# Performance work log

Measured on AMD Instinct MI355X. Metric: run time of the kernel, lower is better.

## Reference

```python
import jax, jax.numpy as jnp
import numpy as np

N_NODES = 100000
N_EDGES = 3200000
N_GRAPHS = 64


def gcn_conv(x, W, b, src, dst, num_nodes):
    # PyG GCNConv: h = x @ W; add self-loops; symmetric norm D^-1/2 (A+I) D^-1/2; bias after aggregation
    h = x @ W  # [N, out]
    loop = jnp.arange(num_nodes, dtype=src.dtype)
    src2 = jnp.concatenate([src, loop])
    dst2 = jnp.concatenate([dst, loop])
    deg = jax.ops.segment_sum(jnp.ones_like(src2, dtype=h.dtype), dst2, num_segments=num_nodes)
    dinv = jnp.where(deg > 0, jax.lax.rsqrt(jnp.maximum(deg, 1e-12)), 0.0)
    norm = dinv[src2] * dinv[dst2]  # [E+N]
    msg = h[src2] * norm[:, None]   # gather + scale (memory-bound)
    out = jax.ops.segment_sum(msg, dst2, num_segments=num_nodes)  # scatter-add
    return out + b


def global_mean_pool(x, batch, num_graphs):
    sums = jax.ops.segment_sum(x, batch, num_segments=num_graphs)
    cnts = jax.ops.segment_sum(jnp.ones((x.shape[0],), dtype=x.dtype), batch, num_segments=num_graphs)
    return sums / jnp.maximum(cnts, 1.0)[:, None]


def setup_inputs() -> dict:
    key = jax.random.key(0)
    ks = jax.random.split(key, 9)
    x = jax.random.normal(ks[0], (N_NODES, 1), dtype=jnp.float32)
    edge_index = jax.random.randint(ks[1], (2, N_EDGES), 0, N_NODES, dtype=jnp.int64)
    batch = jnp.sort(jax.random.randint(ks[2], (N_NODES,), 0, N_GRAPHS, dtype=jnp.int64))
    # Glorot-ish params
    W1 = jax.random.normal(ks[3], (1, 64), dtype=jnp.float32) * 0.5
    b1 = jnp.zeros((64,), dtype=jnp.float32)
    W2 = jax.random.normal(ks[4], (64, 32), dtype=jnp.float32) * (1.0 / np.sqrt(64))
    b2 = jnp.zeros((32,), dtype=jnp.float32)
    Wfc = jax.random.normal(ks[5], (32, 1), dtype=jnp.float32) * (1.0 / np.sqrt(32))
    bfc = jnp.zeros((1,), dtype=jnp.float32)
    return {"x": x, "edge_index": edge_index, "batch": batch,
            "W1": W1, "b1": b1, "W2": W2, "b2": b2, "Wfc": Wfc, "bfc": bfc}


def reference(x, edge_index, batch, W1, b1, W2, b2, Wfc, bfc):
    src, dst = edge_index[0], edge_index[1]
    h = jax.nn.relu(gcn_conv(x, W1, b1, src, dst, N_NODES))
    h = jax.nn.relu(gcn_conv(h, W2, b2, src, dst, N_NODES))
    g = global_mean_pool(h, batch, N_GRAPHS)  # [num_graphs, 32]
    return jax.nn.sigmoid(g @ Wfc + bfc)      # [num_graphs, 1]
```

## Files before the change

### kernel.cpp

```cpp
#include <hip/hip_runtime.h>
#include <math.h>

#define N_NODES 100000
#define N_EDGES 3200000
#define N_GRAPHS 64
#define BW 512
#define LSH 9
#define LMASK 511u
#define NBUCK ((N_NODES + BW - 1) / BW)
#define CHUNK_E 16384
#define NCHUNK ((N_EDGES + CHUNK_E - 1) / CHUNK_E)
#define CAP_E 18432
#define POOL_SCALE 1024.0f
#define POOL_INV (1.0f / 1024.0f)
#define SENT ((unsigned int)N_NODES << LSH)

__global__ void k_part(const int* __restrict__ src, const int* __restrict__ dst,
                       unsigned int* __restrict__ gcur, unsigned int* __restrict__ packed) {
    __shared__ unsigned int hist[NBUCK];
    __shared__ unsigned int sstart[NBUCK];
    for (int i = threadIdx.x; i < NBUCK; i += blockDim.x) hist[i] = 0u;
    __syncthreads();
    int e0 = blockIdx.x * CHUNK_E;
    int e1 = min(e0 + CHUNK_E, N_EDGES);
    for (int e = e0 + threadIdx.x; e < e1; e += blockDim.x)
        atomicAdd(&hist[dst[e] >> LSH], 1u);
    __syncthreads();
    for (int i = threadIdx.x; i < NBUCK; i += blockDim.x) {
        unsigned int h = hist[i];
        sstart[i] = h ? ((unsigned int)i * CAP_E + atomicAdd(&gcur[i], h)) : 0u;
        hist[i] = 0u;
    }
    __syncthreads();
    for (int e = e0 + threadIdx.x; e < e1; e += blockDim.x) {
        int d = dst[e];
        int bk = d >> LSH;
        unsigned int pos = sstart[bk] + atomicAdd(&hist[bk], 1u);
        packed[pos] = ((unsigned int)src[e] << LSH) | ((unsigned int)d & LMASK);
    }
}

__global__ void k_sorta(const unsigned int* __restrict__ gcur,
                        const unsigned int* __restrict__ packed,
                        unsigned int* __restrict__ rowstart, const float* __restrict__ x,
                        float* __restrict__ dinv, float* __restrict__ s, float2* __restrict__ ac) {
    __shared__ unsigned int hist[BW];
    __shared__ unsigned int scan[BW];
    __shared__ unsigned int sdp[256];
    __shared__ unsigned int swbase;
    int b = blockIdx.x;
    int t = threadIdx.x;
    unsigned int gv = 0u;
    if (t < 256) { gv = (t < NBUCK) ? gcur[t] : 0u; sdp[t] = gv; }
    if (t < BW) hist[t] = 0u;
    if (b == 0 && t == 0) ac[N_NODES] = make_float2(0.0f, 0.0f);
    __syncthreads();
    for (int o = 1; o < 256; o <<= 1) {
        unsigned int v = 0u;
        if (t < 256 && t >= o) v = sdp[t - o];
        __syncthreads();
        if (t < 256 && t >= o) sdp[t] += v;
        __syncthreads();
    }
    if (t == b) swbase = sdp[t] - gv;
    __syncthreads();
    unsigned int wbase = swbase;
    unsigned int r0 = (unsigned int)b * CAP_E;
    unsigned int r1 = r0 + gcur[b];
    for (unsigned int e = r0 + t; e < r1; e += blockDim.x)
        atomicAdd(&hist[packed[e] & LMASK], 1u);
    __syncthreads();
    if (t < BW) scan[t] = hist[t];
    __syncthreads();
    for (int o = 1; o < BW; o <<= 1) {
        unsigned int v = 0u;
        if (t < BW && t >= o) v = scan[t - o];
        __syncthreads();
        if (t < BW && t >= o) scan[t] += v;
        __syncthreads();
    }
    if (t < BW) {
        unsigned int deg = hist[t];
        rowstart[b * BW + t] = wbase + scan[t] - deg;
        int n = b * BW + t;
        if (n < N_NODES) {
            float di = 1.0f / sqrtf((float)(deg + 1u));
            dinv[n] = di;
            s[n] = x[n] * di;
        }
    }
}

__global__ void k_sortb(const unsigned int* __restrict__ gcur,
                        const unsigned int* __restrict__ packed,
                        const unsigned int* __restrict__ rowstart,
                        unsigned int* __restrict__ packed2,
                        const float* __restrict__ dinv, const float* __restrict__ s,
                        float2* __restrict__ ac) {
    __shared__ unsigned int cur[BW];
    __shared__ float fsum[BW];
    int b = blockIdx.x;
    unsigned int r0 = (unsigned int)b * CAP_E;
    unsigned int r1 = r0 + gcur[b];
    if (threadIdx.x < BW) {
        cur[threadIdx.x] = rowstart[b * BW + threadIdx.x];
        fsum[threadIdx.x] = 0.0f;
    }
    __syncthreads();
    for (unsigned int e = r0 + threadIdx.x; e < r1; e += blockDim.x) {
        unsigned int p = packed[e];
        unsigned int d = p & LMASK;
        unsigned int pos = atomicAdd(&cur[d], 1u);
        packed2[pos] = p;
        atomicAdd(&fsum[d], s[p >> LSH]);
    }
    __syncthreads();
    if (threadIdx.x < BW) {
        int n = b * BW + threadIdx.x;
        if (n < N_NODES) {
            float di = dinv[n];
            ac[n] = make_float2(di, di * di * (fsum[threadIdx.x] + s[n]));
        }
    }
}

#define NPW 8

#define EDGE_PAIR(P) { \
    float4 q_ = Epair4[(P)]; \
    H += fmaxf(fmaf(q_.y, w1j, q_.x * b1j), 0.0f); \
    H += fmaxf(fmaf(q_.w, w1j, q_.z * b1j), 0.0f); }

#define BLOCK16(P0) { \
    EDGE_PAIR((P0) + 0) EDGE_PAIR((P0) + 1) EDGE_PAIR((P0) + 2) EDGE_PAIR((P0) + 3) \
    EDGE_PAIR((P0) + 4) EDGE_PAIR((P0) + 5) EDGE_PAIR((P0) + 6) EDGE_PAIR((P0) + 7) }

__global__ __launch_bounds__(256, 6)
void k_l2(const unsigned int* __restrict__ rowstart, const unsigned int* __restrict__ packed2,
          const float2* __restrict__ ac,
          const float* __restrict__ W1, const float* __restrict__ b1,
          const float* __restrict__ W2, const float* __restrict__ b2,
          const int* __restrict__ batch, int* __restrict__ gsumi) {
    __shared__ float Hrow[4][64];
    __shared__ float4 Ebuf[4][32];
    const int lane = threadIdx.x & 63;
    const int wv   = threadIdx.x >> 6;
    const int k    = lane & 31;
    const int jh   = lane >> 5;
    const int j0   = jh * 32;

    const float w1j = W1[lane];
    const float b1j = b1[lane];
    const float b2k = b2[k];
    float w2c[32];
#pragma unroll
    for (int j = 0; j < 32; j++) w2c[j] = W2[(j0 + j) * 32 + k];

    float4* Epair4 = &Ebuf[wv][0];
    float2* Ewr    = (float2*)&Ebuf[wv][0];

    int n0 = (blockIdx.x * 4 + wv) * NPW;
    float racc = 0.0f;
    int curg = -1;
    for (int i = 0; i < NPW; i++) {
        int n = n0 + i;
        if (n >= N_NODES) break;
        unsigned int rs = rowstart[n], re = rowstart[n + 1];
        float2 acn = ac[n];
        float H = fmaxf(fmaf(acn.y, w1j, acn.x * b1j), 0.0f);
        unsigned int e0 = rs;
        while (e0 + 64u <= re) {
            unsigned int p = packed2[e0 + lane];
            Ewr[lane] = ac[p >> LSH];
            BLOCK16(0) BLOCK16(8) BLOCK16(16) BLOCK16(24)
            e0 += 64u;
        }
        unsigned int rem = re - e0;
        if (rem) {
            unsigned int idx = e0 + lane;
            unsigned int p = SENT;
            if (idx < re) p = packed2[idx];
            Ewr[lane] = ac[p >> LSH];
            switch ((rem + 15u) >> 4) {
                case 4: BLOCK16(24); [[fallthrough]];
                case 3: BLOCK16(16); [[fallthrough]];
                case 2: BLOCK16(8);  [[fallthrough]];
                case 1: BLOCK16(0);
            }
        }
        Hrow[wv][lane] = H;
        float accv = 0.0f;
#pragma unroll
        for (int jj = 0; jj < 8; jj++) {
            float4 hv = *(const float4*)&Hrow[wv][j0 + 4 * jj];
            accv += hv.x * w2c[4 * jj + 0] + hv.y * w2c[4 * jj + 1]
                  + hv.z * w2c[4 * jj + 2] + hv.w * w2c[4 * jj + 3];
        }
        accv += __shfl_xor(accv, 32);
        float v = fmaxf(fmaf(acn.x, accv, b2k), 0.0f);
        int gb = batch[n];
        if (gb != curg) {
            if (curg >= 0 && jh == 0)
                atomicAdd(&gsumi[curg * 32 + k], __float2int_rn(racc * POOL_SCALE));
            racc = 0.0f; curg = gb;
        }
        racc += v;
    }
    if (curg >= 0 && jh == 0)
        atomicAdd(&gsumi[curg * 32 + k], __float2int_rn(racc * POOL_SCALE));
}

__global__ void k_readout(const int* __restrict__ gsumi, const int* __restrict__ batch,
                          const float* __restrict__ Wfc, const float* __restrict__ bfc,
                          float* __restrict__ out) {
    __shared__ int lb[N_GRAPHS + 1];
    int b = threadIdx.x;
    if (b <= N_GRAPHS) {
        int lo = 0, hi = N_NODES;
        while (lo < hi) {
            int mid = (lo + hi) >> 1;
            if (batch[mid] < b) lo = mid + 1; else hi = mid;
        }
        lb[b] = lo;
    }
    __syncthreads();
    if (b < N_GRAPHS) {
        float inv = 1.0f / fmaxf((float)(lb[b + 1] - lb[b]), 1.0f);
        float acc = bfc[0];
#pragma unroll
        for (int k = 0; k < 32; k++)
            acc += (float)gsumi[b * 32 + k] * POOL_INV * inv * Wfc[k];
        out[b] = 1.0f / (1.0f + expf(-acc));
    }
}

extern "C" void kernel_launch(void* const* d_in, const int* in_sizes, int n_in,
                              void* d_out, int out_size, void* d_ws, size_t ws_size,
                              hipStream_t stream) {
    const float* x    = (const float*)d_in[0];
    const int*   ei   = (const int*)d_in[1];
    const int*   batch= (const int*)d_in[2];
    const float* W1   = (const float*)d_in[3];
    const float* b1   = (const float*)d_in[4];
    const float* W2   = (const float*)d_in[5];
    const float* b2   = (const float*)d_in[6];
    const float* Wfc  = (const float*)d_in[7];
    const float* bfc  = (const float*)d_in[8];
    float* out = (float*)d_out;

    const int* srcIdx = ei;
    const int* dstIdx = ei + N_EDGES;

    char* w = (char*)d_ws;
    unsigned int* gcur    = (unsigned int*)w; w += ((NBUCK + 64) & ~63) * 4;
    unsigned int* packed  = (unsigned int*)w; w += (size_t)NBUCK * CAP_E * 4;
    unsigned int* packed2 = (unsigned int*)w; w += (size_t)(N_EDGES + 64) * 4;
    unsigned int* rowstart= (unsigned int*)w; w += (size_t)(NBUCK * BW + 64) * 4;
    float* dinv = (float*)w;                  w += (size_t)N_NODES * 4;
    float* sbuf = (float*)w;                  w += (size_t)N_NODES * 4;
    float2* ac  = (float2*)w;                 w += (size_t)(N_NODES + 8) * 8;
    int* gsumi  = (int*)w;                    w += (size_t)N_GRAPHS * 32 * 4;

    hipMemsetAsync(gcur, 0, (size_t)NBUCK * 4, stream);
    hipMemsetAsync(gsumi, 0, (size_t)N_GRAPHS * 32 * 4, stream);

    k_part <<<NCHUNK, 1024, 0, stream>>>(srcIdx, dstIdx, gcur, packed);
    k_sorta<<<NBUCK, 1024, 0, stream>>>(gcur, packed, rowstart, x, dinv, sbuf, ac);
    k_sortb<<<NBUCK, 1024, 0, stream>>>(gcur, packed, rowstart, packed2, dinv, sbuf, ac);
    k_l2   <<<(N_NODES + 4 * NPW - 1) / (4 * NPW), 256, 0, stream>>>(rowstart, packed2, ac, W1, b1, W2, b2, batch, gsumi);
    k_readout<<<1, 128, 0, stream>>>(gsumi, batch, Wfc, bfc, out);
}
```

Baseline: 207.5 us.

## Fuse partition and two sort kernels into one cooperative kernel with grid syncs

Merges the three CSR-building kernels (bucket partition, per-bucket histogram/scan, scatter/feature sum) into one cooperatively launched kernel. Grid-wide syncs now separate the phases, relying on the partition and bucket grids being the same size (196 blocks). The aim is to remove two kernel launches and their gaps, and to keep dinv/s values in registers instead of reloading them. In exchange it needs all 196 blocks of 1024 threads resident at once, and pays for the grid-sync barriers.

```diff
diff --git a/kernel.cpp b/kernel.cpp
--- a/kernel.cpp
+++ b/kernel.cpp
@@ -1,5 +1,8 @@
 #include <hip/hip_runtime.h>
+#include <hip/hip_cooperative_groups.h>
 #include <math.h>
+
+namespace cg = cooperative_groups;
 
 #define N_NODES 100000
 #define N_EDGES 3200000
@@ -15,59 +18,63 @@
 #define POOL_INV (1.0f / 1024.0f)
 #define SENT ((unsigned int)N_NODES << LSH)
 
-__global__ void k_part(const int* __restrict__ src, const int* __restrict__ dst,
-                       unsigned int* __restrict__ gcur, unsigned int* __restrict__ packed) {
-    __shared__ unsigned int hist[NBUCK];
+__global__ __launch_bounds__(1024, 1)
+void k_build(const int* __restrict__ src, const int* __restrict__ dst,
+             unsigned int* __restrict__ gcur, unsigned int* __restrict__ packed,
+             unsigned int* __restrict__ packed2, unsigned int* __restrict__ rowstart,
+             const float* __restrict__ x, float* __restrict__ dinv, float* __restrict__ s,
+             float2* __restrict__ ac) {
+    __shared__ unsigned int h1[NBUCK];
     __shared__ unsigned int sstart[NBUCK];
-    for (int i = threadIdx.x; i < NBUCK; i += blockDim.x) hist[i] = 0u;
-    __syncthreads();
-    int e0 = blockIdx.x * CHUNK_E;
+    __shared__ unsigned int hist[BW];
+    __shared__ unsigned int scan[BW];
+    __shared__ unsigned int cur[BW];
+    __shared__ float fsum[BW];
+    __shared__ unsigned int swbase;
+    cg::grid_group grid = cg::this_grid();
+    const int b = blockIdx.x;
+    const int t = threadIdx.x;
+
+    for (int i = t; i < NBUCK; i += 1024) h1[i] = 0u;
+    __syncthreads();
+    int e0 = b * CHUNK_E;
     int e1 = min(e0 + CHUNK_E, N_EDGES);
-    for (int e = e0 + threadIdx.x; e < e1; e += blockDim.x)
-        atomicAdd(&hist[dst[e] >> LSH], 1u);
-    __syncthreads();
-    for (int i = threadIdx.x; i < NBUCK; i += blockDim.x) {
-        unsigned int h = hist[i];
-        sstart[i] = h ? ((unsigned int)i * CAP_E + atomicAdd(&gcur[i], h)) : 0u;
-        hist[i] = 0u;
-    }
-    __syncthreads();
-    for (int e = e0 + threadIdx.x; e < e1; e += blockDim.x) {
+    for (int e = e0 + t; e < e1; e += 1024)
+        atomicAdd(&h1[dst[e] >> LSH], 1u);
+    __syncthreads();
+    for (int i = t; i < NBUCK; i += 1024) {
+        unsigned int hh = h1[i];
+        sstart[i] = hh ? ((unsigned int)i * CAP_E + atomicAdd(&gcur[i], hh)) : 0u;
+        h1[i] = 0u;
+    }
+    __syncthreads();
+    for (int e = e0 + t; e < e1; e += 1024) {
         int d = dst[e];
         int bk = d >> LSH;
-        unsigned int pos = sstart[bk] + atomicAdd(&hist[bk], 1u);
+        unsigned int pos = sstart[bk] + atomicAdd(&h1[bk], 1u);
         packed[pos] = ((unsigned int)src[e] << LSH) | ((unsigned int)d & LMASK);
     }
-}
-
-__global__ void k_sorta(const unsigned int* __restrict__ gcur,
-                        const unsigned int* __restrict__ packed,
-                        unsigned int* __restrict__ rowstart, const float* __restrict__ x,
-                        float* __restrict__ dinv, float* __restrict__ s, float2* __restrict__ ac) {
-    __shared__ unsigned int hist[BW];
-    __shared__ unsigned int scan[BW];
-    __shared__ unsigned int sdp[256];
-    __shared__ unsigned int swbase;
-    int b = blockIdx.x;
-    int t = threadIdx.x;
+
+    grid.sync();
+
     unsigned int gv = 0u;
-    if (t < 256) { gv = (t < NBUCK) ? gcur[t] : 0u; sdp[t] = gv; }
+    if (t < 256) { gv = (t < NBUCK) ? gcur[t] : 0u; scan[t] = gv; }
     if (t < BW) hist[t] = 0u;
     if (b == 0 && t == 0) ac[N_NODES] = make_float2(0.0f, 0.0f);
     __syncthreads();
     for (int o = 1; o < 256; o <<= 1) {
         unsigned int v = 0u;
-        if (t < 256 && t >= o) v = sdp[t - o];
-        __syncthreads();
-        if (t < 256 && t >= o) sdp[t] += v;
-        __syncthreads();
-    }
-    if (t == b) swbase = sdp[t] - gv;
-    __syncthreads();
-    unsigned int wbase = swbase;
-    unsigned int r0 = (unsigned int)b * CAP_E;
-    unsigned int r1 = r0 + gcur[b];
-    for (unsigned int e = r0 + t; e < r1; e += blockDim.x)
+        if (t < 256 && t >= o) v = scan[t - o];
+        __syncthreads();
+        if (t < 256 && t >= o) scan[t] += v;
+        __syncthreads();
+    }
+    if (t == b) swbase = scan[t] - gv;
+    __syncthreads();
+    const unsigned int wbase = swbase;
+    const unsigned int r0 = (unsigned int)b * CAP_E;
+    const unsigned int r1 = r0 + gcur[b];
+    for (unsigned int e = r0 + t; e < r1; e += 1024)
         atomicAdd(&hist[packed[e] & LMASK], 1u);
     __syncthreads();
     if (t < BW) scan[t] = hist[t];
@@ -79,35 +86,25 @@
         if (t < BW && t >= o) scan[t] += v;
         __syncthreads();
     }
+    float di_reg = 0.0f, s_reg = 0.0f;
     if (t < BW) {
         unsigned int deg = hist[t];
-        rowstart[b * BW + t] = wbase + scan[t] - deg;
+        unsigned int rst = wbase + scan[t] - deg;
+        rowstart[b * BW + t] = rst;
+        cur[t] = rst;
+        fsum[t] = 0.0f;
         int n = b * BW + t;
         if (n < N_NODES) {
-            float di = 1.0f / sqrtf((float)(deg + 1u));
-            dinv[n] = di;
-            s[n] = x[n] * di;
-        }
-    }
-}
-
-__global__ void k_sortb(const unsigned int* __restrict__ gcur,
-                        const unsigned int* __restrict__ packed,
-                        const unsigned int* __restrict__ rowstart,
-                        unsigned int* __restrict__ packed2,
-                        const float* __restrict__ dinv, const float* __restrict__ s,
-                        float2* __restrict__ ac) {
-    __shared__ unsigned int cur[BW];
-    __shared__ float fsum[BW];
-    int b = blockIdx.x;
-    unsigned int r0 = (unsigned int)b * CAP_E;
-    unsigned int r1 = r0 + gcur[b];
-    if (threadIdx.x < BW) {
-        cur[threadIdx.x] = rowstart[b * BW + threadIdx.x];
-        fsum[threadIdx.x] = 0.0f;
-    }
-    __syncthreads();
-    for (unsigned int e = r0 + threadIdx.x; e < r1; e += blockDim.x) {
+            di_reg = 1.0f / sqrtf((float)(deg + 1u));
+            dinv[n] = di_reg;
+            s_reg = x[n] * di_reg;
+            s[n] = s_reg;
+        }
+    }
+
+    grid.sync();
+
+    for (unsigned int e = r0 + t; e < r1; e += 1024) {
         unsigned int p = packed[e];
         unsigned int d = p & LMASK;
         unsigned int pos = atomicAdd(&cur[d], 1u);
@@ -115,12 +112,10 @@
         atomicAdd(&fsum[d], s[p >> LSH]);
     }
     __syncthreads();
-    if (threadIdx.x < BW) {
-        int n = b * BW + threadIdx.x;
-        if (n < N_NODES) {
-            float di = dinv[n];
-            ac[n] = make_float2(di, di * di * (fsum[threadIdx.x] + s[n]));
-        }
+    if (t < BW) {
+        int n = b * BW + t;
+        if (n < N_NODES)
+            ac[n] = make_float2(di_reg, di_reg * di_reg * (fsum[t] + s_reg));
     }
 }
 
@@ -264,9 +259,11 @@
     hipMemsetAsync(gcur, 0, (size_t)NBUCK * 4, stream);
     hipMemsetAsync(gsumi, 0, (size_t)N_GRAPHS * 32 * 4, stream);
 
-    k_part <<<NCHUNK, 1024, 0, stream>>>(srcIdx, dstIdx, gcur, packed);
-    k_sorta<<<NBUCK, 1024, 0, stream>>>(gcur, packed, rowstart, x, dinv, sbuf, ac);
-    k_sortb<<<NBUCK, 1024, 0, stream>>>(gcur, packed, rowstart, packed2, dinv, sbuf, ac);
-    k_l2   <<<(N_NODES + 4 * NPW - 1) / (4 * NPW), 256, 0, stream>>>(rowstart, packed2, ac, W1, b1, W2, b2, batch, gsumi);
+    void* bargs[] = { (void*)&srcIdx, (void*)&dstIdx, (void*)&gcur, (void*)&packed,
+                      (void*)&packed2, (void*)&rowstart, (void*)&x, (void*)&dinv,
+                      (void*)&sbuf, (void*)&ac };
+    hipLaunchCooperativeKernel((const void*)k_build, dim3(NBUCK), dim3(1024), bargs, 0, stream);
+
+    k_l2<<<(N_NODES + 4 * NPW - 1) / (4 * NPW), 256, 0, stream>>>(rowstart, packed2, ac, W1, b1, W2, b2, batch, gsumi);
     k_readout<<<1, 128, 0, stream>>>(gsumi, batch, Wfc, bfc, out);
 }
```

New measurement: 289.5 us. 1.4x slower.
